# Kernel tuning notes

Measured on AMD Instinct MI355X. Metric: run time of the kernel, lower is better.

## Reference

```python
import jax, jax.numpy as jnp
import numpy as np

B, T, E, D, H = 4, 1024, 768, 768, 8


def setup_inputs() -> dict:
    key = jax.random.key(0)
    ks = jax.random.split(key, 9)
    s_in = 1.0 / np.sqrt(E)
    s_d = 1.0 / np.sqrt(D)
    x = jax.random.normal(ks[0], (B, T, E), dtype=jnp.float32)
    # Per-head full-width projection weights, stacked over heads.
    # torch Linear stores W as [out,in]; we store as [H, in, out] for einsum.
    wq = jax.random.normal(ks[1], (H, E, D), dtype=jnp.float32) * s_in
    bq = jax.random.normal(ks[2], (H, D), dtype=jnp.float32) * 0.01
    wk = jax.random.normal(ks[3], (H, E, D), dtype=jnp.float32) * s_in
    bk = jax.random.normal(ks[4], (H, D), dtype=jnp.float32) * 0.01
    wv = jax.random.normal(ks[5], (H, E, D), dtype=jnp.float32) * s_in
    bv = jax.random.normal(ks[6], (H, D), dtype=jnp.float32) * 0.01
    wo = jax.random.normal(ks[7], (H, D, E), dtype=jnp.float32) * s_d
    bo = jax.random.normal(ks[8], (H, E), dtype=jnp.float32) * 0.01
    return {"x": x, "wq": wq, "bq": bq, "wk": wk, "bk": bk,
            "wv": wv, "bv": bv, "wo": wo, "bo": bo}


def reference(x, wq, bq, wk, bk, wv, bv, wo, bo):
    # NOTE: original scales by sqrt(dim_emb), not sqrt(dim_internal).
    scale = jnp.float32(1.0 / np.sqrt(E))
    # Batched over heads: q/k/v are [B, H, T, D]
    q = jnp.einsum('bte,hed->bhtd', x, wq) + bq[None, :, None, :]
    k = jnp.einsum('bte,hed->bhtd', x, wk) + bk[None, :, None, :]
    v = jnp.einsum('bte,hed->bhtd', x, wv) + bv[None, :, None, :]
    dot = jnp.einsum('bhtd,bhsd->bhts', q, k) * scale  # [B,H,T,T]
    p_attn = jax.nn.softmax(dot, axis=-1)
    z = jnp.einsum('bhts,bhsd->bhtd', p_attn, v)       # [B,H,T,D]
    # Sum over heads of per-head output projections (+ all head biases)
    out = jnp.einsum('bhtd,hde->bte', z, wo) + jnp.sum(bo, axis=0)[None, None, :]
    return out
```

## Files before the change

kernel.cpp:

```cpp
#include <hip/hip_runtime.h>
#include <hip/hip_bf16.h>


typedef __bf16 bf16x8 __attribute__((ext_vector_type(8)));
typedef float  f32x4  __attribute__((ext_vector_type(4)));
typedef short  s16x4  __attribute__((ext_vector_type(4)));

#define AS1 __attribute__((address_space(1)))
#define AS3 __attribute__((address_space(3)))

__device__ inline void gload_lds16(const void* g, void* l) {
  __builtin_amdgcn_global_load_lds((AS1 const void*)g, (AS3 void*)l, 16, 0, 0);
}

__device__ inline unsigned short f2bf(float f) {
  union { float f; unsigned u; } c; c.f = f;
  unsigned r = c.u + 0x7FFF + ((c.u >> 16) & 1);
  return (unsigned short)(r >> 16);
}
__device__ inline float bf2f(unsigned short u) {
  return __uint_as_float(((unsigned)u) << 16);
}

__device__ inline void swizzle_bid(int& bx, int& by, int& bz) {
  const int gx = gridDim.x, gy = gridDim.y, gz = gridDim.z;
  const int n = gx * gy * gz;
  if ((n & 7) == 0) {
    int lin = (blockIdx.z * gy + blockIdx.y) * gx + blockIdx.x;
    lin = (lin & 7) * (n >> 3) + (lin >> 3);
    bz = lin / (gx * gy);
    const int rem = lin - bz * gx * gy;
    by = rem / gx;
    bx = rem - by * gx;
  } else {
    bx = blockIdx.x; by = blockIdx.y; bz = blockIdx.z;
  }
}

template<bool OUT_F32>
__global__ __launch_bounds__(256, 2)
void gemm_bt_kernel(const unsigned short* __restrict__ A,
                    const unsigned short* __restrict__ Bt,
                    void* __restrict__ Cout,
                    const float* __restrict__ bias,
                    int K, int lda, int ldb,
                    long long aZ, long long bZ,
                    long long cZhi, long long cZlo, int zShift,
                    long long cRowHi, int rowShift, int ldc,
                    long long biasZ, float scale,
                    unsigned short* __restrict__ vtOut,
                    float* __restrict__ rowsumOut,
                    const float* __restrict__ rowScale)
{
  __shared__ unsigned short As[128 * 64];
  __shared__ unsigned short Bs[128 * 64];

  int ntile, mtile, z;
  swizzle_bid(ntile, mtile, z);

  const int tid  = threadIdx.x;
  const int wave = tid >> 6;
  const int lane = tid & 63;
  const int wm = wave >> 1, wn = wave & 1;

  const unsigned short* Ab = A  + (size_t)z * aZ + (size_t)mtile * 128 * lda;
  const unsigned short* Bb = Bt + (size_t)z * bZ + (size_t)ntile * 128 * ldb;

  const int rlane = lane >> 3;
  const int su    = ((lane & 7) ^ rlane) * 8;

  const int rsel  = lane & 15;
  const int usel  = lane & 7;
  const int ubase = lane >> 4;
  const int koff0 = ((ubase) ^ usel) * 8;
  const int koff1 = ((4 | ubase) ^ usel) * 8;

  f32x4 acc[4][4] = {};

  const int nkt = K >> 6;
  for (int kt = 0; kt < nkt; ++kt) {
    const int kbase = kt * 64;
    __syncthreads();
#pragma unroll
    for (int i = 0; i < 4; ++i) {
      const int r = wave * 32 + i * 8;
      gload_lds16(Ab + (size_t)(r + rlane) * lda + kbase + su, &As[r * 64]);
      gload_lds16(Bb + (size_t)(r + rlane) * ldb + kbase + su, &Bs[r * 64]);
    }
    __syncthreads();
#pragma unroll
    for (int kk = 0; kk < 2; ++kk) {
      const int koff = kk ? koff1 : koff0;
      bf16x8 af[4], bfr[4];
#pragma unroll
      for (int f = 0; f < 4; ++f) {
        af[f]  = *(const bf16x8*)&As[(wm * 64 + f * 16 + rsel) * 64 + koff];
        bfr[f] = *(const bf16x8*)&Bs[(wn * 64 + f * 16 + rsel) * 64 + koff];
      }
#pragma unroll
      for (int fm = 0; fm < 4; ++fm)
#pragma unroll
        for (int fn = 0; fn < 4; ++fn)
          acc[fm][fn] = __builtin_amdgcn_mfma_f32_16x16x32_bf16(af[fm], bfr[fn], acc[fm][fn], 0, 0, 0);
    }
  }

  if (vtOut && z >= 16) {
    const long long hoff = (long long)(z - 16) * 786432LL;
#pragma unroll
    for (int fm = 0; fm < 4; ++fm) {
#pragma unroll
      for (int fn = 0; fn < 4; ++fn) {
        const int n  = ntile * 128 + wn * 64 + fn * 16 + (lane & 15);
        const int m0 = mtile * 128 + wm * 64 + fm * 16 + (lane >> 4) * 4;
        const int b  = m0 >> 10, t0 = m0 & 1023;
        const float bb = bias ? bias[(size_t)z * biasZ + n] : 0.f;
        s16x4 w;
#pragma unroll
        for (int j = 0; j < 4; ++j)
          w[j] = (short)f2bf(acc[fm][fn][j] * scale + bb);
        *(s16x4*)&vtOut[(size_t)b * 6291456 + hoff + (size_t)n * 1024 + t0] = w;
      }
    }
    return;
  }

  const long long zoff = (long long)(z >> zShift) * cZhi
                       + (long long)(z & ((1 << zShift) - 1)) * cZlo;

  if (rowsumOut) {
    __syncthreads();
    float* redsum = (float*)As;
#pragma unroll
    for (int fm = 0; fm < 4; ++fm) {
#pragma unroll
      for (int j = 0; j < 4; ++j) {
        const int m = mtile * 128 + wm * 64 + fm * 16 + (lane >> 4) * 4 + j;
        const long long rowoff = (long long)(m >> rowShift) * cRowHi
                               + (long long)(m & ((1 << rowShift) - 1)) * ldc;
        float part = 0.f;
#pragma unroll
        for (int fn = 0; fn < 4; ++fn) {
          const int n = ntile * 128 + wn * 64 + fn * 16 + (lane & 15);
          const float e = __expf(acc[fm][fn][j] * scale);
          part += e;
          ((unsigned short*)Cout)[zoff + rowoff + n] = f2bf(e);
        }
#pragma unroll
        for (int o = 1; o < 16; o <<= 1) part += __shfl_xor(part, o);
        if ((lane & 15) == 0)
          redsum[(wm * 64 + fm * 16 + (lane >> 4) * 4 + j) * 2 + wn] = part;
      }
    }
    __syncthreads();
    if (tid < 128) {
      const int m = mtile * 128 + tid;
      rowsumOut[((long long)z * 8 + ntile) * 1024 + m] =
          redsum[tid * 2 + 0] + redsum[tid * 2 + 1];
    }
    return;
  }

#pragma unroll
  for (int fm = 0; fm < 4; ++fm) {
#pragma unroll
    for (int j = 0; j < 4; ++j) {
      const int m = mtile * 128 + wm * 64 + fm * 16 + (lane >> 4) * 4 + j;
      const long long rowoff = (long long)(m >> rowShift) * cRowHi
                             + (long long)(m & ((1 << rowShift) - 1)) * ldc;
      const float rsc = rowScale ? rowScale[(size_t)z * 1024 + (m & 1023)] : 1.0f;
#pragma unroll
      for (int fn = 0; fn < 4; ++fn) {
        const int n = ntile * 128 + wn * 64 + fn * 16 + (lane & 15);
        float v = acc[fm][fn][j] * scale;
        if (bias) v += bias[(size_t)z * biasZ + n];
        v *= rsc;
        const long long cidx = zoff + rowoff + n;
        if (OUT_F32) ((float*)Cout)[cidx] = v;
        else ((unsigned short*)Cout)[cidx] = f2bf(v);
      }
    }
  }
}

__global__ void prep_weights_kernel(const float* __restrict__ wq,
                                    const float* __restrict__ wk,
                                    const float* __restrict__ wv,
                                    const float* __restrict__ wo,
                                    unsigned short* __restrict__ wqkvT,
                                    unsigned short* __restrict__ woT)
{
  __shared__ float tile[32][33];
  const int z = blockIdx.z;
  const float* in;
  unsigned short* outp;
  int outLD;
  if (z < 24) {
    const float* base = (z < 8) ? wq : (z < 16) ? wk : wv;
    in   = base + (size_t)(z & 7) * 589824;
    outp = wqkvT + (size_t)z * 589824;
    outLD = 768;
  } else {
    in   = wo + (size_t)(z - 24) * 589824;
    outp = woT + (size_t)(z - 24) * 768;
    outLD = 6144;
  }
  const int c0 = blockIdx.x * 32, r0 = blockIdx.y * 32;
  const int tx = threadIdx.x, ty = threadIdx.y;
#pragma unroll
  for (int i = ty; i < 32; i += 8)
    tile[i][tx] = in[(size_t)(r0 + i) * 768 + c0 + tx];
  __syncthreads();
#pragma unroll
  for (int i = ty; i < 32; i += 8)
    outp[(size_t)(c0 + i) * outLD + r0 + tx] = f2bf(tile[tx][i]);
}

__global__ void transpose_conv_kernel(const float* __restrict__ in,
                                      unsigned short* __restrict__ out,
                                      int R, int C)
{
  __shared__ float tile[32][33];
  const size_t zo = (size_t)blockIdx.z * R * C;
  const int c0 = blockIdx.x * 32, r0 = blockIdx.y * 32;
  const int tx = threadIdx.x, ty = threadIdx.y;
#pragma unroll
  for (int i = ty; i < 32; i += 8)
    tile[i][tx] = in[zo + (size_t)(r0 + i) * C + c0 + tx];
  __syncthreads();
#pragma unroll
  for (int i = ty; i < 32; i += 8)
    out[zo + (size_t)(c0 + i) * R + r0 + tx] = f2bf(tile[tx][i]);
}

__global__ void transpose_bf16_kernel(const unsigned short* __restrict__ in,
                                      unsigned short* __restrict__ out,
                                      int R, int C)
{
  __shared__ unsigned short tile[32][33];
  const size_t zo = (size_t)blockIdx.z * R * C;
  const int c0 = blockIdx.x * 32, r0 = blockIdx.y * 32;
  const int tx = threadIdx.x, ty = threadIdx.y;
#pragma unroll
  for (int i = ty; i < 32; i += 8)
    tile[i][tx] = in[zo + (size_t)(r0 + i) * C + c0 + tx];
  __syncthreads();
#pragma unroll
  for (int i = ty; i < 32; i += 8)
    out[zo + (size_t)(c0 + i) * R + r0 + tx] = tile[tx][i];
}

__global__ void convert_f32_bf16_kernel(const float* __restrict__ in,
                                        unsigned short* __restrict__ out, int n4)
{
  const int i = blockIdx.x * blockDim.x + threadIdx.x;
  if (i < n4) {
    const float4 f = ((const float4*)in)[i];
    s16x4 o;
    o[0] = (short)f2bf(f.x); o[1] = (short)f2bf(f.y);
    o[2] = (short)f2bf(f.z); o[3] = (short)f2bf(f.w);
    ((s16x4*)out)[i] = o;
  }
}

__global__ void bosum_kernel(const float* __restrict__ bo, float* __restrict__ bos)
{
  const int e = blockIdx.x * blockDim.x + threadIdx.x;
  if (e < 768) {
    float s = 0.f;
#pragma unroll
    for (int h = 0; h < 8; ++h) s += bo[h * 768 + e];
    bos[e] = s;
  }
}

__global__ void bconcat_kernel(const float* __restrict__ bq,
                               const float* __restrict__ bk,
                               const float* __restrict__ bv,
                               float* __restrict__ bqkv)
{
  const int i = blockIdx.x * blockDim.x + threadIdx.x;
  if (i < 24 * 768) {
    const int z = i / 768, d = i - z * 768;
    const float* src = (z < 8) ? bq : (z < 16) ? bk : bv;
    bqkv[i] = src[(z & 7) * 768 + d];
  }
}

__global__ void invden_kernel(const float* __restrict__ rowsum,
                              float* __restrict__ invden)
{
  const int i = blockIdx.x * blockDim.x + threadIdx.x;
  if (i < 32 * 1024) {
    const int z = i >> 10, t = i & 1023;
    const float* p = rowsum + (size_t)z * 8192 + t;
    float s = 0.f;
#pragma unroll
    for (int nt = 0; nt < 8; ++nt) s += p[nt * 1024];
    invden[i] = 1.0f / s;
  }
}

__global__ void reduce4_kernel(const float* __restrict__ partials,
                               const float* __restrict__ bos,
                               float* __restrict__ out, int n4)
{
  const int i = blockIdx.x * blockDim.x + threadIdx.x;
  if (i < n4) {
    const long long stride4 = 4096LL * 768 / 4;
    float4 a = ((const float4*)partials)[i];
    float4 b = ((const float4*)partials)[i + stride4];
    float4 c = ((const float4*)partials)[i + 2 * stride4];
    float4 d = ((const float4*)partials)[i + 3 * stride4];
    const int col = (i * 4) % 768;
    const float4 b4 = *(const float4*)&bos[col];
    float4 r;
    r.x = a.x + b.x + c.x + d.x + b4.x;
    r.y = a.y + b.y + c.y + d.y + b4.y;
    r.z = a.z + b.z + c.z + d.z + b4.z;
    r.w = a.w + b.w + c.w + d.w + b4.w;
    ((float4*)out)[i] = r;
  }
}

__global__ __launch_bounds__(256)
void softmax_kernel(unsigned short* __restrict__ S)
{
  const size_t row = blockIdx.x;
  unsigned short* p = S + row * 1024;
  const int t = threadIdx.x;

  s16x4 raw = *((const s16x4*)p + t);
  float v[4];
#pragma unroll
  for (int j = 0; j < 4; ++j) v[j] = bf2f((unsigned short)raw[j]);

  float mx = fmaxf(fmaxf(v[0], v[1]), fmaxf(v[2], v[3]));
#pragma unroll
  for (int o = 1; o < 64; o <<= 1) mx = fmaxf(mx, __shfl_xor(mx, o));

  __shared__ float red[8];
  if ((t & 63) == 0) red[t >> 6] = mx;
  __syncthreads();
  mx = fmaxf(fmaxf(red[0], red[1]), fmaxf(red[2], red[3]));

  float e[4], s = 0.f;
#pragma unroll
  for (int j = 0; j < 4; ++j) { e[j] = __expf(v[j] - mx); s += e[j]; }
#pragma unroll
  for (int o = 1; o < 64; o <<= 1) s += __shfl_xor(s, o);
  if ((t & 63) == 0) red[4 + (t >> 6)] = s;
  __syncthreads();
  s = red[4] + red[5] + red[6] + red[7];
  const float inv = 1.0f / s;

  s16x4 outv;
#pragma unroll
  for (int j = 0; j < 4; ++j) outv[j] = (short)f2bf(e[j] * inv);
  *((s16x4*)p + t) = outv;
}

extern "C" void kernel_launch(void* const* d_in, const int* in_sizes, int n_in,
                              void* d_out, int out_size, void* d_ws, size_t ws_size,
                              hipStream_t stream)
{
  (void)in_sizes; (void)n_in; (void)out_size;
  constexpr int Bb = 4, T = 1024, E = 768, D = 768, H = 8;
  constexpr int HD = H * D;
  constexpr long long TD = (long long)T * D;
  constexpr long long TT = (long long)T * T;
  constexpr long long DE = (long long)D * E;
  constexpr long long DT = (long long)D * T;
  constexpr long long BHTD = (long long)Bb * H * T * D;
  constexpr long long HTD = (long long)H * TD;
  constexpr float SCALE = 0.03608439182435161f;

  const float* x  = (const float*)d_in[0];
  const float* wq = (const float*)d_in[1];
  const float* bq = (const float*)d_in[2];
  const float* wk = (const float*)d_in[3];
  const float* bk = (const float*)d_in[4];
  const float* wv = (const float*)d_in[5];
  const float* bv = (const float*)d_in[6];
  const float* wo = (const float*)d_in[7];
  const float* bo = (const float*)d_in[8];
  float* out = (float*)d_out;

  unsigned char* wsb = (unsigned char*)d_ws;
  const dim3 tb32(32, 8);

  if (ws_size >= 245443584ULL + 4096ULL) {
    unsigned short* woT   = (unsigned short*)(wsb + 0);
    float*          bos   = (float*)(wsb + 9437184);
    float*          bqkv  = (float*)(wsb + 9440256);
    unsigned short* vT    = (unsigned short*)(wsb + 9513984);
    unsigned short* qkv   = (unsigned short*)(wsb + 59845632);
    unsigned short* q     = qkv;
    unsigned short* k     = qkv + BHTD;
    unsigned short* xb    = (unsigned short*)(wsb + 210840576);
    unsigned short* wqkvT = (unsigned short*)(wsb + 217132032);
    unsigned short* S     = qkv + 2 * BHTD;
    float*          part  = (float*)k;
    unsigned short* z2    = q;
    float*          rowsum = (float*)(wsb + 227617792);
    float*          invden = (float*)(wsb + 228666368);

    convert_f32_bf16_kernel<<<3072, 256, 0, stream>>>(x, xb, Bb * T * E / 4);
    prep_weights_kernel<<<dim3(24, 24, 32), tb32, 0, stream>>>(
        wq, wk, wv, wo, wqkvT, woT);
    bosum_kernel<<<3, 256, 0, stream>>>(bo, bos);
    bconcat_kernel<<<72, 256, 0, stream>>>(bq, bk, bv, bqkv);

    gemm_bt_kernel<false><<<dim3(6, 32, 24), 256, 0, stream>>>(
        xb, wqkvT, qkv, bqkv, E, E, E,
        0LL, DE, BHTD, TD, 3, HTD, 10, D, 768LL, 1.0f, vT, nullptr, nullptr);

    gemm_bt_kernel<false><<<dim3(8, 8, 32), 256, 0, stream>>>(
        q, k, S, nullptr, D, D, D,
        TD, TD, TT, 0LL, 0, 0LL, 30, T, 0LL, SCALE, nullptr, rowsum, nullptr);

    invden_kernel<<<128, 256, 0, stream>>>(rowsum, invden);

    gemm_bt_kernel<false><<<dim3(6, 8, 32), 256, 0, stream>>>(
        S, vT, z2, nullptr, T, T, T,
        TT, DT, (long long)T * HD, (long long)D, 3, 0LL, 30, HD, 0LL, 1.0f,
        nullptr, nullptr, invden);

    gemm_bt_kernel<true><<<dim3(6, 32, 4), 256, 0, stream>>>(
        z2, woT, part, nullptr, 1536, HD, HD,
        1536LL, 1536LL, 3145728LL, 0LL, 0, 0LL, 30, E, 0LL, 1.0f,
        nullptr, nullptr, nullptr);
    reduce4_kernel<<<3072, 256, 0, stream>>>(part, bos, out, 4096 * 768 / 4);
    return;
  }

  const size_t FIXED = 84937728ULL;
  const size_t PERCH = 8388608ULL;
  int CH = 8;
  while (CH > 1 && FIXED + (size_t)CH * PERCH > ws_size) CH >>= 1;

  size_t off = 0;
  auto carve = [&](size_t bytes) -> void* {
    void* p = wsb + off;
    off += (bytes + 255) & ~(size_t)255;
    return p;
  };
  unsigned short* xb  = (unsigned short*)carve((size_t)Bb * T * E * 2);
  unsigned short* wqT = (unsigned short*)carve((size_t)H * D * E * 2);
  unsigned short* wkT = (unsigned short*)carve((size_t)H * D * E * 2);
  unsigned short* wvT = (unsigned short*)carve((size_t)H * D * E * 2);
  float*          bos = (float*)carve(E * 4);
  unsigned short* z2  = (unsigned short*)carve((size_t)Bb * T * HD * 2);
  unsigned short* qc  = (unsigned short*)carve((size_t)CH * T * D * 2);
  unsigned short* kc  = (unsigned short*)carve((size_t)CH * T * D * 2);
  unsigned short* vc  = (unsigned short*)carve((size_t)CH * T * D * 2);
  unsigned short* vTc = (unsigned short*)carve((size_t)CH * D * T * 2);
  unsigned short* Sc  = (unsigned short*)carve((size_t)CH * T * T * 2);
  unsigned short* woT = wqT;

  convert_f32_bf16_kernel<<<3072, 256, 0, stream>>>(x, xb, Bb * T * E / 4);
  transpose_conv_kernel<<<dim3(24, 24, 8), tb32, 0, stream>>>(wq, wqT, E, D);
  transpose_conv_kernel<<<dim3(24, 24, 8), tb32, 0, stream>>>(wk, wkT, E, D);
  transpose_conv_kernel<<<dim3(24, 24, 8), tb32, 0, stream>>>(wv, wvT, E, D);
  bosum_kernel<<<3, 256, 0, stream>>>(bo, bos);

  const int nchunks = (Bb * H) / CH;
  for (int c = 0; c < nchunks; ++c) {
    const int z0 = c * CH;
    const int b  = z0 >> 3;
    const int h0 = z0 & 7;
    const unsigned short* xbb = xb + (size_t)b * T * E;

    gemm_bt_kernel<false><<<dim3(6, 8, CH), 256, 0, stream>>>(
        xbb, wqT + (size_t)h0 * DE, qc, bq + (size_t)h0 * D, E, E, E,
        0LL, DE, TD, 0LL, 0, 0LL, 30, D, (long long)D, 1.0f,
        nullptr, nullptr, nullptr);
    gemm_bt_kernel<false><<<dim3(6, 8, CH), 256, 0, stream>>>(
        xbb, wkT + (size_t)h0 * DE, kc, bk + (size_t)h0 * D, E, E, E,
        0LL, DE, TD, 0LL, 0, 0LL, 30, D, (long long)D, 1.0f,
        nullptr, nullptr, nullptr);
    gemm_bt_kernel<false><<<dim3(6, 8, CH), 256, 0, stream>>>(
        xbb, wvT + (size_t)h0 * DE, vc, bv + (size_t)h0 * D, E, E, E,
        0LL, DE, TD, 0LL, 0, 0LL, 30, D, (long long)D, 1.0f,
        nullptr, nullptr, nullptr);

    transpose_bf16_kernel<<<dim3(24, 32, CH), tb32, 0, stream>>>(vc, vTc, T, D);

    gemm_bt_kernel<false><<<dim3(8, 8, CH), 256, 0, stream>>>(
        qc, kc, Sc, nullptr, D, D, D,
        TD, TD, TT, 0LL, 0, 0LL, 30, T, 0LL, SCALE,
        nullptr, nullptr, nullptr);

    softmax_kernel<<<CH * T, 256, 0, stream>>>(Sc);

    gemm_bt_kernel<false><<<dim3(6, 8, CH), 256, 0, stream>>>(
        Sc, vTc, z2 + (size_t)b * T * HD + (size_t)h0 * D, nullptr, T, T, T,
        TT, DT, (long long)D, 0LL, 0, 0LL, 30, HD, 0LL, 1.0f,
        nullptr, nullptr, nullptr);
  }

  transpose_conv_kernel<<<dim3(24, 192, 1), tb32, 0, stream>>>(wo, woT, HD, E);
  gemm_bt_kernel<true><<<dim3(6, 32, 1), 256, 0, stream>>>(
      z2, woT, out, bos, HD, HD, HD,
      0LL, 0LL, 0LL, 0LL, 0, 0LL, 30, E, 0LL, 1.0f,
      nullptr, nullptr, nullptr);
}
```

Measured before the change: 356.1 us.

## Add 256x256-tile 8-wave GEMM kernel for QKV projection and QK^T scores

Adds a new GEMM kernel with 256x256 output tiles, 512 threads, 128KB dynamic LDS, double-buffered direct-to-LDS loads, and MFMA phases interleaved with prefetch and priority bumps. It replaces the older kernel for the QKV projection (with V-transpose epilogue) and for the scores GEMM (with exp/rowsum epilogue); invden now takes a variable tile count. The larger tiles raise operand reuse and cut global traffic, at the cost of fewer blocks, lower occupancy and heavy register pressure. There is a fallback if the shared memory attribute cannot be set.

```diff
diff --git a/kernel.cpp b/kernel.cpp
--- a/kernel.cpp
+++ b/kernel.cpp
@@ -34,6 +34,234 @@
     bx = rem - by * gx;
   } else {
     bx = blockIdx.x; by = blockIdx.y; bz = blockIdx.z;
+  }
+}
+
+__device__ __forceinline__ void stage2_256(const unsigned short* __restrict__ G,
+                                           int ld, int kbase,
+                                           unsigned short* lbase,
+                                           int tid, int wave, int cc0) {
+  const int sr = tid >> 3;
+  const int su = (tid & 7) ^ ((tid >> 3) & 7);
+#pragma unroll
+  for (int cc = cc0; cc < cc0 + 2; ++cc)
+    gload_lds16(G + (size_t)(cc * 64 + sr) * ld + kbase + su * 8,
+                lbase + (cc * 64 + wave * 8) * 64);
+}
+
+#define LGK0_PIN() do { \
+    asm volatile("s_waitcnt lgkmcnt(0)" ::: "memory"); \
+    __builtin_amdgcn_sched_barrier(0); } while (0)
+
+template<int MODE>
+__global__ __launch_bounds__(512, 2)
+void gemm256_kernel(const unsigned short* __restrict__ A,
+                    const unsigned short* __restrict__ Bt,
+                    void* __restrict__ Cout,
+                    const float* __restrict__ bias,
+                    int K, int lda, int ldb,
+                    long long aZ, long long bZ,
+                    long long cZhi, long long cZlo, int zShift,
+                    long long cRowHi, int rowShift, int ldc,
+                    long long biasZ, float scale,
+                    unsigned short* __restrict__ vtOut,
+                    float* __restrict__ rowsumOut)
+{
+  extern __shared__ unsigned short sm[];
+
+  int ntile, mtile, z;
+  swizzle_bid(ntile, mtile, z);
+
+  const int tid  = threadIdx.x;
+  const int wave = tid >> 6;
+  const int lane = tid & 63;
+  const int wm = wave >> 2, wn = wave & 3;
+
+  const unsigned short* Ab = A  + (size_t)z * aZ + (size_t)mtile * 256 * lda;
+  const unsigned short* Bb = Bt + (size_t)z * bZ + (size_t)ntile * 256 * ldb;
+
+  const int rsel  = lane & 15;
+  const int usel  = lane & 7;
+  const int ubase = lane >> 4;
+  const int koff0 = ((ubase) ^ usel) * 8;
+  const int koff1 = ((4 | ubase) ^ usel) * 8;
+
+  f32x4 acc[8][4] = {};
+
+  const int nkt = K >> 6;
+  stage2_256(Ab, lda, 0, sm, tid, wave, 0);
+  stage2_256(Ab, lda, 0, sm, tid, wave, 2);
+  stage2_256(Bb, ldb, 0, sm + 16384, tid, wave, 0);
+  stage2_256(Bb, ldb, 0, sm + 16384, tid, wave, 2);
+  if (nkt > 1) {
+    stage2_256(Bb, ldb, 64, sm + 32768 + 16384, tid, wave, 0);
+    stage2_256(Bb, ldb, 64, sm + 32768 + 16384, tid, wave, 2);
+    asm volatile("s_waitcnt vmcnt(4)" ::: "memory");
+  } else {
+    asm volatile("s_waitcnt vmcnt(0)" ::: "memory");
+  }
+  __builtin_amdgcn_sched_barrier(0);
+  __builtin_amdgcn_s_barrier();
+
+  for (int t = 0; t < nkt; ++t) {
+    const unsigned short* Ac = sm + (t & 1) * 32768;
+    const unsigned short* Bc = Ac + 16384;
+    unsigned short* An = sm + ((t + 1) & 1) * 32768;
+    unsigned short* Bn = sm + (t & 1) * 32768 + 16384;
+    const int kb1 = (t + 1) * 64, kb2 = (t + 2) * 64;
+    bf16x8 a[4], b0[4], b1[4];
+
+#pragma unroll
+    for (int f = 0; f < 4; ++f) {
+      b0[f] = *(const bf16x8*)&Bc[(wn * 64 + f * 16 + rsel) * 64 + koff0];
+      a[f]  = *(const bf16x8*)&Ac[(wm * 128 + f * 16 + rsel) * 64 + koff0];
+    }
+    __builtin_amdgcn_sched_barrier(0);
+    if (t + 1 < nkt) stage2_256(Ab, lda, kb1, An, tid, wave, 0);
+    __builtin_amdgcn_sched_barrier(0);
+    __builtin_amdgcn_s_barrier();
+    LGK0_PIN();
+    __builtin_amdgcn_s_setprio(1);
+#pragma unroll
+    for (int fm = 0; fm < 4; ++fm)
+#pragma unroll
+      for (int fn = 0; fn < 4; ++fn)
+        acc[fm][fn] = __builtin_amdgcn_mfma_f32_16x16x32_bf16(a[fm], b0[fn], acc[fm][fn], 0, 0, 0);
+    __builtin_amdgcn_s_setprio(0);
+    __builtin_amdgcn_sched_barrier(0);
+    __builtin_amdgcn_s_barrier();
+
+#pragma unroll
+    for (int f = 0; f < 4; ++f)
+      a[f] = *(const bf16x8*)&Ac[(wm * 128 + 64 + f * 16 + rsel) * 64 + koff0];
+    __builtin_amdgcn_sched_barrier(0);
+    if (t + 1 < nkt) stage2_256(Ab, lda, kb1, An, tid, wave, 2);
+    __builtin_amdgcn_sched_barrier(0);
+    __builtin_amdgcn_s_barrier();
+    LGK0_PIN();
+    __builtin_amdgcn_s_setprio(1);
+#pragma unroll
+    for (int fm = 0; fm < 4; ++fm)
+#pragma unroll
+      for (int fn = 0; fn < 4; ++fn)
+        acc[4 + fm][fn] = __builtin_amdgcn_mfma_f32_16x16x32_bf16(a[fm], b0[fn], acc[4 + fm][fn], 0, 0, 0);
+    __builtin_amdgcn_s_setprio(0);
+    __builtin_amdgcn_sched_barrier(0);
+    __builtin_amdgcn_s_barrier();
+
+#pragma unroll
+    for (int f = 0; f < 4; ++f) {
+      b1[f] = *(const bf16x8*)&Bc[(wn * 64 + f * 16 + rsel) * 64 + koff1];
+      a[f]  = *(const bf16x8*)&Ac[(wm * 128 + f * 16 + rsel) * 64 + koff1];
+    }
+    __builtin_amdgcn_sched_barrier(0);
+    __builtin_amdgcn_s_barrier();
+    LGK0_PIN();
+    __builtin_amdgcn_s_setprio(1);
+#pragma unroll
+    for (int fm = 0; fm < 4; ++fm)
+#pragma unroll
+      for (int fn = 0; fn < 4; ++fn)
+        acc[fm][fn] = __builtin_amdgcn_mfma_f32_16x16x32_bf16(a[fm], b1[fn], acc[fm][fn], 0, 0, 0);
+    __builtin_amdgcn_s_setprio(0);
+    __builtin_amdgcn_sched_barrier(0);
+    __builtin_amdgcn_s_barrier();
+
+#pragma unroll
+    for (int f = 0; f < 4; ++f)
+      a[f] = *(const bf16x8*)&Ac[(wm * 128 + 64 + f * 16 + rsel) * 64 + koff1];
+    __builtin_amdgcn_sched_barrier(0);
+    if (t + 2 < nkt) {
+      stage2_256(Bb, ldb, kb2, Bn, tid, wave, 0);
+      stage2_256(Bb, ldb, kb2, Bn, tid, wave, 2);
+      asm volatile("s_waitcnt vmcnt(4)" ::: "memory");
+    } else {
+      asm volatile("s_waitcnt vmcnt(0)" ::: "memory");
+    }
+    __builtin_amdgcn_sched_barrier(0);
+    __builtin_amdgcn_s_barrier();
+    LGK0_PIN();
+    __builtin_amdgcn_s_setprio(1);
+#pragma unroll
+    for (int fm = 0; fm < 4; ++fm)
+#pragma unroll
+      for (int fn = 0; fn < 4; ++fn)
+        acc[4 + fm][fn] = __builtin_amdgcn_mfma_f32_16x16x32_bf16(a[fm], b1[fn], acc[4 + fm][fn], 0, 0, 0);
+    __builtin_amdgcn_s_setprio(0);
+    __builtin_amdgcn_sched_barrier(0);
+    __builtin_amdgcn_s_barrier();
+  }
+
+  if (MODE == 1 && z >= 16) {
+    const long long hoff = (long long)(z - 16) * 786432LL;
+#pragma unroll
+    for (int fm = 0; fm < 8; ++fm) {
+#pragma unroll
+      for (int fn = 0; fn < 4; ++fn) {
+        const int n  = ntile * 256 + wn * 64 + fn * 16 + (lane & 15);
+        const int m0 = mtile * 256 + wm * 128 + fm * 16 + (lane >> 4) * 4;
+        const int b  = m0 >> 10, t0 = m0 & 1023;
+        const float bb = bias ? bias[(size_t)z * biasZ + n] : 0.f;
+        s16x4 w;
+#pragma unroll
+        for (int j = 0; j < 4; ++j)
+          w[j] = (short)f2bf(acc[fm][fn][j] * scale + bb);
+        *(s16x4*)&vtOut[(size_t)b * 6291456 + hoff + (size_t)n * 1024 + t0] = w;
+      }
+    }
+    return;
+  }
+
+  const long long zoff = (long long)(z >> zShift) * cZhi
+                       + (long long)(z & ((1 << zShift) - 1)) * cZlo;
+
+  if (MODE == 2) {
+    __syncthreads();
+    float* redsum = (float*)sm;
+#pragma unroll
+    for (int fm = 0; fm < 8; ++fm) {
+#pragma unroll
+      for (int j = 0; j < 4; ++j) {
+        const int rl = wm * 128 + fm * 16 + (lane >> 4) * 4 + j;
+        const int m  = mtile * 256 + rl;
+        const long long rowoff = (long long)(m >> rowShift) * cRowHi
+                               + (long long)(m & ((1 << rowShift) - 1)) * ldc;
+        float part = 0.f;
+#pragma unroll
+        for (int fn = 0; fn < 4; ++fn) {
+          const int n = ntile * 256 + wn * 64 + fn * 16 + (lane & 15);
+          const float e = __expf(acc[fm][fn][j] * scale);
+          part += e;
+          ((unsigned short*)Cout)[zoff + rowoff + n] = f2bf(e);
+        }
+#pragma unroll
+        for (int o = 1; o < 16; o <<= 1) part += __shfl_xor(part, o);
+        if ((lane & 15) == 0) redsum[rl * 4 + wn] = part;
+      }
+    }
+    __syncthreads();
+    if (tid < 256) {
+      rowsumOut[((long long)z * 4 + ntile) * 1024 + mtile * 256 + tid] =
+          redsum[tid * 4] + redsum[tid * 4 + 1] + redsum[tid * 4 + 2] + redsum[tid * 4 + 3];
+    }
+    return;
+  }
+
+#pragma unroll
+  for (int fm = 0; fm < 8; ++fm) {
+#pragma unroll
+    for (int j = 0; j < 4; ++j) {
+      const int m = mtile * 256 + wm * 128 + fm * 16 + (lane >> 4) * 4 + j;
+      const long long rowoff = (long long)(m >> rowShift) * cRowHi
+                             + (long long)(m & ((1 << rowShift) - 1)) * ldc;
+#pragma unroll
+      for (int fn = 0; fn < 4; ++fn) {
+        const int n = ntile * 256 + wn * 64 + fn * 16 + (lane & 15);
+        float v = acc[fm][fn][j] * scale;
+        if (bias) v += bias[(size_t)z * biasZ + n];
+        ((unsigned short*)Cout)[zoff + rowoff + n] = f2bf(v);
+      }
+    }
   }
 }
 
@@ -288,15 +516,14 @@
 }
 
 __global__ void invden_kernel(const float* __restrict__ rowsum,
-                              float* __restrict__ invden)
+                              float* __restrict__ invden, int NT)
 {
   const int i = blockIdx.x * blockDim.x + threadIdx.x;
   if (i < 32 * 1024) {
     const int z = i >> 10, t = i & 1023;
-    const float* p = rowsum + (size_t)z * 8192 + t;
+    const float* p = rowsum + (size_t)z * NT * 1024 + t;
     float s = 0.f;
-#pragma unroll
-    for (int nt = 0; nt < 8; ++nt) s += p[nt * 1024];
+    for (int nt = 0; nt < NT; ++nt) s += p[nt * 1024];
     invden[i] = 1.0f / s;
   }
 }
@@ -389,6 +616,14 @@
   unsigned char* wsb = (unsigned char*)d_ws;
   const dim3 tb32(32, 8);
 
+  bool use256 = true;
+  if (hipFuncSetAttribute(reinterpret_cast<const void*>(gemm256_kernel<1>),
+                          hipFuncAttributeMaxDynamicSharedMemorySize, 131072)
+      != hipSuccess) use256 = false;
+  if (hipFuncSetAttribute(reinterpret_cast<const void*>(gemm256_kernel<2>),
+                          hipFuncAttributeMaxDynamicSharedMemorySize, 131072)
+      != hipSuccess) use256 = false;
+
   if (ws_size >= 245443584ULL + 4096ULL) {
     unsigned short* woT   = (unsigned short*)(wsb + 0);
     float*          bos   = (float*)(wsb + 9437184);
@@ -411,15 +646,23 @@
     bosum_kernel<<<3, 256, 0, stream>>>(bo, bos);
     bconcat_kernel<<<72, 256, 0, stream>>>(bq, bk, bv, bqkv);
 
-    gemm_bt_kernel<false><<<dim3(6, 32, 24), 256, 0, stream>>>(
-        xb, wqkvT, qkv, bqkv, E, E, E,
-        0LL, DE, BHTD, TD, 3, HTD, 10, D, 768LL, 1.0f, vT, nullptr, nullptr);
-
-    gemm_bt_kernel<false><<<dim3(8, 8, 32), 256, 0, stream>>>(
-        q, k, S, nullptr, D, D, D,
-        TD, TD, TT, 0LL, 0, 0LL, 30, T, 0LL, SCALE, nullptr, rowsum, nullptr);
-
-    invden_kernel<<<128, 256, 0, stream>>>(rowsum, invden);
+    if (use256) {
+      gemm256_kernel<1><<<dim3(3, 16, 24), 512, 131072, stream>>>(
+          xb, wqkvT, qkv, bqkv, E, E, E,
+          0LL, DE, BHTD, TD, 3, HTD, 10, D, 768LL, 1.0f, vT, nullptr);
+      gemm256_kernel<2><<<dim3(4, 4, 32), 512, 131072, stream>>>(
+          q, k, S, nullptr, D, D, D,
+          TD, TD, TT, 0LL, 0, 0LL, 30, T, 0LL, SCALE, nullptr, rowsum);
+      invden_kernel<<<128, 256, 0, stream>>>(rowsum, invden, 4);
+    } else {
+      gemm_bt_kernel<false><<<dim3(6, 32, 24), 256, 0, stream>>>(
+          xb, wqkvT, qkv, bqkv, E, E, E,
+          0LL, DE, BHTD, TD, 3, HTD, 10, D, 768LL, 1.0f, vT, nullptr, nullptr);
+      gemm_bt_kernel<false><<<dim3(8, 8, 32), 256, 0, stream>>>(
+          q, k, S, nullptr, D, D, D,
+          TD, TD, TT, 0LL, 0, 0LL, 30, T, 0LL, SCALE, nullptr, rowsum, nullptr);
+      invden_kernel<<<128, 256, 0, stream>>>(rowsum, invden, 8);
+    }
 
     gemm_bt_kernel<false><<<dim3(6, 8, 32), 256, 0, stream>>>(
         S, vT, z2, nullptr, T, T, T,
```

New measurement: 411.6 us. 1.16x slower.

## Fold output projection into value weights by precomputing Wv·Wo per head

Applied to the files above, without the earlier changes.

Precomputes per-head fused weights Wv_h·Wo_h (with a new bias bv·Wo), so the V projection directly produces the value times the output projection. This removes the separate z-times-Wo GEMM: the PV GEMM now writes fp32 per-head partials that an 8-way reduction sums with the output bias. The cost is an extra 8×768³ weight-prep GEMM on every call, a larger fp32 partial buffer and 8-way reduction traffic, plus extra bf16 rounding of the fused weights.

```diff
diff --git a/kernel.cpp b/kernel.cpp
--- a/kernel.cpp
+++ b/kernel.cpp
@@ -48,7 +48,8 @@
                     long long cZhi, long long cZlo, int zShift,
                     long long cRowHi, int rowShift, int ldc,
                     long long biasZ, float scale,
-                    unsigned short* __restrict__ vtOut,
+                    unsigned short* __restrict__ ctOut, int ctZmin,
+                    long long ctZ, long long ctRowHi, int ctLdc,
                     float* __restrict__ rowsumOut,
                     const float* __restrict__ rowScale)
 {
@@ -105,21 +106,21 @@
     }
   }
 
-  if (vtOut && z >= 16) {
-    const long long hoff = (long long)(z - 16) * 786432LL;
+  if (ctOut && z >= ctZmin) {
+    const long long zo = (long long)(z & 7) * ctZ;
 #pragma unroll
     for (int fm = 0; fm < 4; ++fm) {
 #pragma unroll
       for (int fn = 0; fn < 4; ++fn) {
         const int n  = ntile * 128 + wn * 64 + fn * 16 + (lane & 15);
         const int m0 = mtile * 128 + wm * 64 + fm * 16 + (lane >> 4) * 4;
-        const int b  = m0 >> 10, t0 = m0 & 1023;
         const float bb = bias ? bias[(size_t)z * biasZ + n] : 0.f;
         s16x4 w;
 #pragma unroll
         for (int j = 0; j < 4; ++j)
           w[j] = (short)f2bf(acc[fm][fn][j] * scale + bb);
-        *(s16x4*)&vtOut[(size_t)b * 6291456 + hoff + (size_t)n * 1024 + t0] = w;
+        *(s16x4*)&ctOut[zo + (long long)(m0 >> 10) * ctRowHi + (m0 & 1023)
+                        + (long long)n * ctLdc] = w;
       }
     }
     return;
@@ -185,25 +186,21 @@
 
 __global__ void prep_weights_kernel(const float* __restrict__ wq,
                                     const float* __restrict__ wk,
-                                    const float* __restrict__ wv,
                                     const float* __restrict__ wo,
                                     unsigned short* __restrict__ wqkvT,
-                                    unsigned short* __restrict__ woT)
+                                    unsigned short* __restrict__ woTh)
 {
   __shared__ float tile[32][33];
   const int z = blockIdx.z;
   const float* in;
   unsigned short* outp;
-  int outLD;
-  if (z < 24) {
-    const float* base = (z < 8) ? wq : (z < 16) ? wk : wv;
+  if (z < 16) {
+    const float* base = (z < 8) ? wq : wk;
     in   = base + (size_t)(z & 7) * 589824;
     outp = wqkvT + (size_t)z * 589824;
-    outLD = 768;
   } else {
-    in   = wo + (size_t)(z - 24) * 589824;
-    outp = woT + (size_t)(z - 24) * 768;
-    outLD = 6144;
+    in   = wo + (size_t)(z - 16) * 589824;
+    outp = woTh + (size_t)(z - 16) * 589824;
   }
   const int c0 = blockIdx.x * 32, r0 = blockIdx.y * 32;
   const int tx = threadIdx.x, ty = threadIdx.y;
@@ -213,7 +210,7 @@
   __syncthreads();
 #pragma unroll
   for (int i = ty; i < 32; i += 8)
-    outp[(size_t)(c0 + i) * outLD + r0 + tx] = f2bf(tile[tx][i]);
+    outp[(size_t)(c0 + i) * 768 + r0 + tx] = f2bf(tile[tx][i]);
 }
 
 __global__ void transpose_conv_kernel(const float* __restrict__ in,
@@ -274,15 +271,28 @@
   }
 }
 
+__global__ void bvo_kernel(const float* __restrict__ bv,
+                           const float* __restrict__ wo,
+                           float* __restrict__ bvo)
+{
+  const int h = blockIdx.z;
+  const int e2 = blockIdx.x * 256 + threadIdx.x;
+  const float* wob = wo + (size_t)h * 589824;
+  const float* bvb = bv + (size_t)h * 768;
+  float s = 0.f;
+  for (int d = 0; d < 768; ++d) s += bvb[d] * wob[(size_t)d * 768 + e2];
+  bvo[(size_t)h * 768 + e2] = s;
+}
+
 __global__ void bconcat_kernel(const float* __restrict__ bq,
                                const float* __restrict__ bk,
-                               const float* __restrict__ bv,
+                               const float* __restrict__ bvo,
                                float* __restrict__ bqkv)
 {
   const int i = blockIdx.x * blockDim.x + threadIdx.x;
   if (i < 24 * 768) {
     const int z = i / 768, d = i - z * 768;
-    const float* src = (z < 8) ? bq : (z < 16) ? bk : bv;
+    const float* src = (z < 8) ? bq : (z < 16) ? bk : bvo;
     bqkv[i] = src[(z & 7) * 768 + d];
   }
 }
@@ -301,25 +311,23 @@
   }
 }
 
-__global__ void reduce4_kernel(const float* __restrict__ partials,
+__global__ void reduce8_kernel(const float* __restrict__ partials,
                                const float* __restrict__ bos,
                                float* __restrict__ out, int n4)
 {
   const int i = blockIdx.x * blockDim.x + threadIdx.x;
   if (i < n4) {
     const long long stride4 = 4096LL * 768 / 4;
-    float4 a = ((const float4*)partials)[i];
-    float4 b = ((const float4*)partials)[i + stride4];
-    float4 c = ((const float4*)partials)[i + 2 * stride4];
-    float4 d = ((const float4*)partials)[i + 3 * stride4];
+    float4 s = ((const float4*)partials)[i];
+#pragma unroll
+    for (int k2 = 1; k2 < 8; ++k2) {
+      float4 p = ((const float4*)partials)[i + k2 * stride4];
+      s.x += p.x; s.y += p.y; s.z += p.z; s.w += p.w;
+    }
     const int col = (i * 4) % 768;
     const float4 b4 = *(const float4*)&bos[col];
-    float4 r;
-    r.x = a.x + b.x + c.x + d.x + b4.x;
-    r.y = a.y + b.y + c.y + d.y + b4.y;
-    r.z = a.z + b.z + c.z + d.z + b4.z;
-    r.w = a.w + b.w + c.w + d.w + b4.w;
-    ((float4*)out)[i] = r;
+    s.x += b4.x; s.y += b4.y; s.z += b4.z; s.w += b4.w;
+    ((float4*)out)[i] = s;
   }
 }
 
@@ -370,7 +378,6 @@
   constexpr long long TD = (long long)T * D;
   constexpr long long TT = (long long)T * T;
   constexpr long long DE = (long long)D * E;
-  constexpr long long DT = (long long)D * T;
   constexpr long long BHTD = (long long)Bb * H * T * D;
   constexpr long long HTD = (long long)H * TD;
   constexpr float SCALE = 0.03608439182435161f;
@@ -390,47 +397,59 @@
   const dim3 tb32(32, 8);
 
   if (ws_size >= 245443584ULL + 4096ULL) {
-    unsigned short* woT   = (unsigned short*)(wsb + 0);
+    unsigned short* woTh  = (unsigned short*)(wsb + 0);
     float*          bos   = (float*)(wsb + 9437184);
     float*          bqkv  = (float*)(wsb + 9440256);
-    unsigned short* vT    = (unsigned short*)(wsb + 9513984);
-    unsigned short* qkv   = (unsigned short*)(wsb + 59845632);
-    unsigned short* q     = qkv;
-    unsigned short* k     = qkv + BHTD;
-    unsigned short* xb    = (unsigned short*)(wsb + 210840576);
-    unsigned short* wqkvT = (unsigned short*)(wsb + 217132032);
-    unsigned short* S     = qkv + 2 * BHTD;
-    float*          part  = (float*)k;
-    unsigned short* z2    = q;
-    float*          rowsum = (float*)(wsb + 227617792);
-    float*          invden = (float*)(wsb + 228666368);
+    float*          bvo   = (float*)(wsb + 9513984);
+    unsigned short* vT    = (unsigned short*)(wsb + 9538560 + 793088);
+    vT = (unsigned short*)(wsb + 9513984 + 262144);
+    unsigned short* qkv   = (unsigned short*)(wsb + 59845632 + 262144);
+    vT = (unsigned short*)(wsb + 9538560);
+    unsigned short* q    = (unsigned short*)(wsb + 59870208);
+    unsigned short* k    = q + BHTD;
+    float*          part = (float*)q;
+    unsigned short* S    = (unsigned short*)(wsb + 160533504);
+    unsigned short* wvb  = (unsigned short*)(wsb + 160533504);
+    float*          rowsum = (float*)(wsb + 227642368);
+    float*          invden = (float*)(wsb + 228690944);
+    unsigned short* xb     = (unsigned short*)(wsb + 228822016);
+    unsigned short* wqkvT  = (unsigned short*)(wsb + 235113472);
+    wvb   = (unsigned short*)(wsb + 160533504);
+    wqkvT = (unsigned short*)(wsb + 160533504 + 9437184);
+    qkv = q;  (void)qkv;
 
     convert_f32_bf16_kernel<<<3072, 256, 0, stream>>>(x, xb, Bb * T * E / 4);
-    prep_weights_kernel<<<dim3(24, 24, 32), tb32, 0, stream>>>(
-        wq, wk, wv, wo, wqkvT, woT);
+    convert_f32_bf16_kernel<<<(int)(H * DE / 4 + 255) / 256, 256, 0, stream>>>(
+        wv, wvb, H * DE / 4);
+    prep_weights_kernel<<<dim3(24, 24, 24), tb32, 0, stream>>>(
+        wq, wk, wo, wqkvT, woTh);
     bosum_kernel<<<3, 256, 0, stream>>>(bo, bos);
-    bconcat_kernel<<<72, 256, 0, stream>>>(bq, bk, bv, bqkv);
+    bvo_kernel<<<dim3(3, 1, 8), 256, 0, stream>>>(bv, wo, bvo);
+    bconcat_kernel<<<72, 256, 0, stream>>>(bq, bk, bvo, bqkv);
+
+    gemm_bt_kernel<false><<<dim3(6, 6, 8), 256, 0, stream>>>(
+        wvb, woTh, nullptr, nullptr, 768, 768, 768,
+        DE, DE, 0LL, 0LL, 30, 0LL, 30, 0, 0LL, 1.0f,
+        wqkvT + 16 * DE, 0, DE, 0LL, 768, nullptr, nullptr);
 
     gemm_bt_kernel<false><<<dim3(6, 32, 24), 256, 0, stream>>>(
-        xb, wqkvT, qkv, bqkv, E, E, E,
-        0LL, DE, BHTD, TD, 3, HTD, 10, D, 768LL, 1.0f, vT, nullptr, nullptr);
+        xb, wqkvT, q, bqkv, E, E, E,
+        0LL, DE, BHTD, TD, 3, HTD, 10, D, 768LL, 1.0f,
+        vT, 16, TD, HTD, 1024, nullptr, nullptr);
 
     gemm_bt_kernel<false><<<dim3(8, 8, 32), 256, 0, stream>>>(
         q, k, S, nullptr, D, D, D,
-        TD, TD, TT, 0LL, 0, 0LL, 30, T, 0LL, SCALE, nullptr, rowsum, nullptr);
+        TD, TD, TT, 0LL, 0, 0LL, 30, T, 0LL, SCALE,
+        nullptr, 0, 0LL, 0LL, 0, rowsum, nullptr);
 
     invden_kernel<<<128, 256, 0, stream>>>(rowsum, invden);
 
-    gemm_bt_kernel<false><<<dim3(6, 8, 32), 256, 0, stream>>>(
-        S, vT, z2, nullptr, T, T, T,
-        TT, DT, (long long)T * HD, (long long)D, 3, 0LL, 30, HD, 0LL, 1.0f,
-        nullptr, nullptr, invden);
-
-    gemm_bt_kernel<true><<<dim3(6, 32, 4), 256, 0, stream>>>(
-        z2, woT, part, nullptr, 1536, HD, HD,
-        1536LL, 1536LL, 3145728LL, 0LL, 0, 0LL, 30, E, 0LL, 1.0f,
-        nullptr, nullptr, nullptr);
-    reduce4_kernel<<<3072, 256, 0, stream>>>(part, bos, out, 4096 * 768 / 4);
+    gemm_bt_kernel<true><<<dim3(6, 8, 32), 256, 0, stream>>>(
+        S, vT, part, nullptr, T, T, T,
+        TT, TD, 786432LL, 3145728LL, 3, 0LL, 30, E, 0LL, 1.0f,
+        nullptr, 0, 0LL, 0LL, 0, nullptr, invden);
+
+    reduce8_kernel<<<3072, 256, 0, stream>>>(part, bos, out, 4096 * 768 / 4);
     return;
   }
 
@@ -464,6 +483,7 @@
   transpose_conv_kernel<<<dim3(24, 24, 8), tb32, 0, stream>>>(wv, wvT, E, D);
   bosum_kernel<<<3, 256, 0, stream>>>(bo, bos);
 
+  constexpr long long DT = (long long)D * T;
   const int nchunks = (Bb * H) / CH;
   for (int c = 0; c < nchunks; ++c) {
     const int z0 = c * CH;
@@ -474,34 +494,34 @@
     gemm_bt_kernel<false><<<dim3(6, 8, CH), 256, 0, stream>>>(
         xbb, wqT + (size_t)h0 * DE, qc, bq + (size_t)h0 * D, E, E, E,
         0LL, DE, TD, 0LL, 0, 0LL, 30, D, (long long)D, 1.0f,
-        nullptr, nullptr, nullptr);
+        nullptr, 0, 0LL, 0LL, 0, nullptr, nullptr);
     gemm_bt_kernel<false><<<dim3(6, 8, CH), 256, 0, stream>>>(
         xbb, wkT + (size_t)h0 * DE, kc, bk + (size_t)h0 * D, E, E, E,
         0LL, DE, TD, 0LL, 0, 0LL, 30, D, (long long)D, 1.0f,
-        nullptr, nullptr, nullptr);
+        nullptr, 0, 0LL, 0LL, 0, nullptr, nullptr);
     gemm_bt_kernel<false><<<dim3(6, 8, CH), 256, 0, stream>>>(
         xbb, wvT + (size_t)h0 * DE, vc, bv + (size_t)h0 * D, E, E, E,
         0LL, DE, TD, 0LL, 0, 0LL, 30, D, (long long)D, 1.0f,
-        nullptr, nullptr, nullptr);
+        nullptr, 0, 0LL, 0LL, 0, nullptr, nullptr);
 
     transpose_bf16_kernel<<<dim3(24, 32, CH), tb32, 0, stream>>>(vc, vTc, T, D);
 
     gemm_bt_kernel<false><<<dim3(8, 8, CH), 256, 0, stream>>>(
         qc, kc, Sc, nullptr, D, D, D,
         TD, TD, TT, 0LL, 0, 0LL, 30, T, 0LL, SCALE,
-        nullptr, nullptr, nullptr);
+        nullptr, 0, 0LL, 0LL, 0, nullptr, nullptr);
 
     softmax_kernel<<<CH * T, 256, 0, stream>>>(Sc);
 
     gemm_bt_kernel<false><<<dim3(6, 8, CH), 256, 0, stream>>>(
         Sc, vTc, z2 + (size_t)b * T * HD + (size_t)h0 * D, nullptr, T, T, T,
         TT, DT, (long long)D, 0LL, 0, 0LL, 30, HD, 0LL, 1.0f,
-        nullptr, nullptr, nullptr);
+        nullptr, 0, 0LL, 0LL, 0, nullptr, nullptr);
   }
 
   transpose_conv_kernel<<<dim3(24, 192, 1), tb32, 0, stream>>>(wo, woT, HD, E);
   gemm_bt_kernel<true><<<dim3(6, 32, 1), 256, 0, stream>>>(
       z2, woT, out, bos, HD, HD, HD,
       0LL, 0LL, 0LL, 0LL, 0, 0LL, 30, E, 0LL, 1.0f,
-      nullptr, nullptr, nullptr);
-}
+      nullptr, 0, 0LL, 0LL, 0, nullptr, nullptr);
+}
```

Result: slower. 391.1 us (+9.8%).
